# Performance work log

Hardware: AMD Instinct MI355X
Metric: run time of the kernel (lower is better)

Reference implementation:

```python
import jax, jax.numpy as jnp
import numpy as np

N = 100000      # total nodes across the batch of graphs
E = 1600000     # total edges (avg degree 16)
D = 128         # dim_drug (== num_feature here)
L = 3           # layer_drug
G = 2048        # number of graphs in the batch
BN_EPS = 1e-5


def setup_inputs() -> dict:
    key = jax.random.key(0)
    ks = jax.random.split(key, 10)
    x = jax.random.normal(ks[0], (N, D), dtype=jnp.float32)
    edge_index = jax.random.randint(ks[1], (2, E), 0, N, dtype=jnp.int64)
    batch = jnp.sort(jax.random.randint(ks[2], (N,), 0, G, dtype=jnp.int64))
    s = 0.05
    W1 = jax.random.normal(ks[3], (L, D, D), dtype=jnp.float32) * s
    b1 = jax.random.normal(ks[4], (L, D), dtype=jnp.float32) * s
    W2 = jax.random.normal(ks[5], (L, D, D), dtype=jnp.float32) * s
    b2 = jax.random.normal(ks[6], (L, D), dtype=jnp.float32) * s
    gamma = jnp.ones((L, D), dtype=jnp.float32)
    beta = jnp.zeros((L, D), dtype=jnp.float32)
    return {"x": x, "edge_index": edge_index, "batch": batch,
            "W1": W1, "b1": b1, "W2": W2, "b2": b2,
            "gamma": gamma, "beta": beta}


def reference(x, edge_index, batch, W1, b1, W2, b2, gamma, beta):
    src, dst = edge_index[0], edge_index[1]
    h = x
    layer_outs = []
    for i in range(L):
        # GINConv, eps=0: MLP( (1+eps)*h + sum_{j->i} h_j )
        agg = jax.ops.segment_sum(h[src], dst, num_segments=N)  # [N, D]
        m = agg + h
        m = jax.nn.relu(m @ W1[i] + b1[i]) @ W2[i] + b2[i]       # 2-layer MLP
        m = jax.nn.relu(m)                                        # F.relu after conv
        # BatchNorm1d (training mode: batch stats over node dim, biased var)
        mean = jnp.mean(m, axis=0)
        var = jnp.mean((m - mean) ** 2, axis=0)
        h = gamma[i] * (m - mean) * jax.lax.rsqrt(var + BN_EPS) + beta[i]
        layer_outs.append(h)
    node_rep = jnp.concatenate(layer_outs, axis=1)  # JK 'cat' -> [N, L*D]
    return jax.ops.segment_max(node_rep, batch, num_segments=G)  # [G, L*D]
```

## Files before the change

kernel.cpp:

```cpp
#include <hip/hip_runtime.h>
#include <stdint.h>

#define NN 100000
#define NE 1600000
#define DD 128
#define NL 3
#define NG 2048
#define BN_EPS 1e-5f
#define CAP 56
#define NXCD 8
#define WIN 12500

typedef short s16x8 __attribute__((ext_vector_type(8)));
typedef float f32x4 __attribute__((ext_vector_type(4)));

__device__ __forceinline__ unsigned short f2bfu(float f) {
    union { float f; unsigned int i; } x; x.f = f;
    unsigned int r = x.i + 0x7fffu + ((x.i >> 16) & 1u);
    return (unsigned short)(r >> 16);
}
__device__ __forceinline__ float bfu2f(unsigned short u) {
    union { unsigned int i; float f; } x; x.i = ((unsigned int)u) << 16; return x.f;
}
__device__ __forceinline__ float uplo(unsigned int u) {
    union { unsigned int i; float f; } x; x.i = u << 16; return x.f;
}
__device__ __forceinline__ float uphi(unsigned int u) {
    union { unsigned int i; float f; } x; x.i = u & 0xffff0000u; return x.f;
}
__device__ __forceinline__ void add8(float* a, uint4 v) {
    a[0] += uplo(v.x); a[1] += uphi(v.x);
    a[2] += uplo(v.y); a[3] += uphi(v.y);
    a[4] += uplo(v.z); a[5] += uphi(v.z);
    a[6] += uplo(v.w); a[7] += uphi(v.w);
}
__device__ __forceinline__ unsigned int pack2(float a, float b) {
    return (unsigned int)f2bfu(a) | ((unsigned int)f2bfu(b) << 16);
}

__global__ __launch_bounds__(256) void k_cvt(
    const float* __restrict__ x, unsigned short* __restrict__ hb)
{
    int i = (blockIdx.x * 256 + threadIdx.x) * 4;
    if (i >= NN * DD) return;
    float4 v = *(const float4*)(x + i);
    ushort4 o;
    o.x = f2bfu(v.x); o.y = f2bfu(v.y); o.z = f2bfu(v.z); o.w = f2bfu(v.w);
    *(ushort4*)(hb + i) = o;
}

__global__ __launch_bounds__(256) void k_wtrans(
    const float* __restrict__ W1, const float* __restrict__ W2,
    unsigned short* __restrict__ Wt)
{
    int idx = blockIdx.x * 256 + threadIdx.x;
    if (idx >= 6 * DD * DD) return;
    int mat = idx >> 14;
    int r = idx & 16383;
    int n = r >> 7, k = r & 127;
    const float* src = (mat < 3) ? (W1 + mat * DD * DD) : (W2 + (mat - 3) * DD * DD);
    Wt[idx] = f2bfu(src[k * DD + n]);
}

__global__ __launch_bounds__(256) void k_bounds(
    const int* __restrict__ batch, int* __restrict__ start)
{
    int n = blockIdx.x * 256 + threadIdx.x;
    if (n >= NN) return;
    int bn = batch[n];
    bn = bn < 0 ? 0 : (bn > NG - 1 ? NG - 1 : bn);
    int bp;
    if (n == 0) bp = -1;
    else {
        bp = batch[n - 1];
        bp = bp < 0 ? 0 : (bp > NG - 1 ? NG - 1 : bp);
    }
    for (int g = bp + 1; g <= bn; ++g) start[g] = n;
    if (n == NN - 1) {
        for (int g = bn + 1; g <= NG; ++g) start[g] = NN;
    }
}

__global__ __launch_bounds__(256) void k_fill2(
    const int* __restrict__ ei, int* __restrict__ cnt, int* __restrict__ csr)
{
    const int xcd = blockIdx.x & 7;
    const int slice = blockIdx.x >> 3;
    const int wlo = xcd * WIN, whi = wlo + WIN;
    int e0 = (slice * 256 + threadIdx.x) * 4;
    if (e0 >= NE) return;
    int4 d4 = *(const int4*)(ei + NE + e0);
    int dd[4] = {d4.x, d4.y, d4.z, d4.w};
    bool any = false;
    #pragma unroll
    for (int i = 0; i < 4; ++i)
        any |= (dd[i] >= wlo && dd[i] < whi);
    if (!any) return;
    int4 s4 = *(const int4*)(ei + e0);
    int ss[4] = {s4.x, s4.y, s4.z, s4.w};
    #pragma unroll
    for (int i = 0; i < 4; ++i) {
        int src = ss[i], dst = dd[i];
        if (dst < wlo || dst >= whi) continue;
        if ((unsigned)src >= NN) continue;
        int pos = atomicAdd(&cnt[dst], 1);
        if (pos < CAP) csr[dst * CAP + pos] = src;
    }
}

__global__ __launch_bounds__(256) void k_agg(
    const unsigned short* __restrict__ hb, const int* __restrict__ cnt,
    const int* __restrict__ csr, unsigned short* __restrict__ aggf)
{
    const int node = blockIdx.x * 16 + (threadIdx.x >> 4);
    const int lane = threadIdx.x & 15;
    if (node >= NN) return;
    int deg = cnt[node];
    deg = deg > CAP ? CAP : deg;
    const int* bkt = csr + node * CAP;
    const unsigned short* base = hb + lane * 8;
    float acc[8];
    {
        uint4 v = *(const uint4*)(base + (long long)node * DD);
        acc[0] = uplo(v.x); acc[1] = uphi(v.x);
        acc[2] = uplo(v.y); acc[3] = uphi(v.y);
        acc[4] = uplo(v.z); acc[5] = uphi(v.z);
        acc[6] = uplo(v.w); acc[7] = uphi(v.w);
    }
    int e = 0;
    for (; e + 4 <= deg; e += 4) {
        int s0 = bkt[e], s1 = bkt[e + 1], s2 = bkt[e + 2], s3 = bkt[e + 3];
        uint4 v0 = *(const uint4*)(base + (long long)s0 * DD);
        uint4 v1 = *(const uint4*)(base + (long long)s1 * DD);
        uint4 v2 = *(const uint4*)(base + (long long)s2 * DD);
        uint4 v3 = *(const uint4*)(base + (long long)s3 * DD);
        add8(acc, v0); add8(acc, v1); add8(acc, v2); add8(acc, v3);
    }
    for (; e < deg; ++e) {
        uint4 v = *(const uint4*)(base + (long long)bkt[e] * DD);
        add8(acc, v);
    }
    uint4 o;
    o.x = pack2(acc[0], acc[1]);
    o.y = pack2(acc[2], acc[3]);
    o.z = pack2(acc[4], acc[5]);
    o.w = pack2(acc[6], acc[7]);
    *(uint4*)(aggf + (long long)node * DD + lane * 8) = o;
}

__global__ __launch_bounds__(256, 2) void k_mlp(
    const unsigned short* __restrict__ aggf, unsigned short* __restrict__ hb,
    const unsigned short* __restrict__ W1t, const float* __restrict__ b1,
    const unsigned short* __restrict__ W2t, const float* __restrict__ b2,
    float* __restrict__ stats)
{
    __shared__ unsigned short lA[128 * 136];
    __shared__ unsigned short lW[128 * 136];
    __shared__ float sSum[4][128];
    __shared__ float sSq[4][128];
    const int tid = threadIdx.x;
    const int row0 = blockIdx.x * 128;

    #pragma unroll
    for (int it = 0; it < 8; ++it) {
        int eidx = (it * 256 + tid) * 8;
        int r = eidx >> 7, c = eidx & 127;
        *(uint4*)(&lW[r * 136 + c]) = *(const uint4*)(W1t + eidx);
    }
    {
        int col8 = tid & 15, rr = tid >> 4;
        #pragma unroll
        for (int it = 0; it < 8; ++it) {
            int r = rr + it * 16;
            int grow = row0 + r;
            uint4 v;
            if (grow < NN) {
                v = *(const uint4*)(aggf + (long long)grow * DD + col8 * 8);
            } else {
                v.x = v.y = v.z = v.w = 0;
            }
            *(uint4*)(&lA[r * 136 + col8 * 8]) = v;
        }
    }
    __syncthreads();

    const int wave = tid >> 6, lane = tid & 63;
    const int quad = lane >> 4, m16 = lane & 15;

    f32x4 acc[2][8] = {};
    #pragma unroll
    for (int k0 = 0; k0 < 128; k0 += 32) {
        const int kk = k0 + quad * 8;
        s16x8 a0 = *(const s16x8*)(&lA[(wave * 32 + m16) * 136 + kk]);
        s16x8 a1 = *(const s16x8*)(&lA[(wave * 32 + 16 + m16) * 136 + kk]);
        #pragma unroll
        for (int ct = 0; ct < 8; ++ct) {
            s16x8 bf = *(const s16x8*)(&lW[(ct * 16 + m16) * 136 + kk]);
            acc[0][ct] = __builtin_amdgcn_mfma_f32_16x16x32_bf16(a0, bf, acc[0][ct], 0, 0, 0);
            acc[1][ct] = __builtin_amdgcn_mfma_f32_16x16x32_bf16(a1, bf, acc[1][ct], 0, 0, 0);
        }
    }
    __syncthreads();

    #pragma unroll
    for (int rt = 0; rt < 2; ++rt) {
        #pragma unroll
        for (int ct = 0; ct < 8; ++ct) {
            int col = ct * 16 + m16;
            float b = b1[col];
            #pragma unroll
            for (int r = 0; r < 4; ++r) {
                int lrow = wave * 32 + rt * 16 + quad * 4 + r;
                lA[lrow * 136 + col] = f2bfu(fmaxf(acc[rt][ct][r] + b, 0.0f));
            }
        }
    }
    #pragma unroll
    for (int it = 0; it < 8; ++it) {
        int eidx = (it * 256 + tid) * 8;
        int r = eidx >> 7, c = eidx & 127;
        *(uint4*)(&lW[r * 136 + c]) = *(const uint4*)(W2t + eidx);
    }
    __syncthreads();

    #pragma unroll
    for (int rt = 0; rt < 2; ++rt)
        #pragma unroll
        for (int ct = 0; ct < 8; ++ct)
            acc[rt][ct] = f32x4{0.f, 0.f, 0.f, 0.f};
    #pragma unroll
    for (int k0 = 0; k0 < 128; k0 += 32) {
        const int kk = k0 + quad * 8;
        s16x8 a0 = *(const s16x8*)(&lA[(wave * 32 + m16) * 136 + kk]);
        s16x8 a1 = *(const s16x8*)(&lA[(wave * 32 + 16 + m16) * 136 + kk]);
        #pragma unroll
        for (int ct = 0; ct < 8; ++ct) {
            s16x8 bf = *(const s16x8*)(&lW[(ct * 16 + m16) * 136 + kk]);
            acc[0][ct] = __builtin_amdgcn_mfma_f32_16x16x32_bf16(a0, bf, acc[0][ct], 0, 0, 0);
            acc[1][ct] = __builtin_amdgcn_mfma_f32_16x16x32_bf16(a1, bf, acc[1][ct], 0, 0, 0);
        }
    }

    float csum[8] = {}, csq[8] = {};
    #pragma unroll
    for (int rt = 0; rt < 2; ++rt) {
        int rbase = row0 + wave * 32 + rt * 16 + quad * 4;
        #pragma unroll
        for (int ct = 0; ct < 8; ++ct) {
            int col = ct * 16 + m16;
            float b = b2[col];
            #pragma unroll
            for (int r = 0; r < 4; ++r) {
                int row = rbase + r;
                if (row < NN) {
                    float v = fmaxf(acc[rt][ct][r] + b, 0.0f);
                    hb[(long long)row * DD + col] = f2bfu(v);
                    csum[ct] += v;
                    csq[ct] += v * v;
                }
            }
        }
    }
    #pragma unroll
    for (int ct = 0; ct < 8; ++ct) {
        csum[ct] += __shfl_xor(csum[ct], 16);
        csum[ct] += __shfl_xor(csum[ct], 32);
        csq[ct]  += __shfl_xor(csq[ct], 16);
        csq[ct]  += __shfl_xor(csq[ct], 32);
    }
    if (quad == 0) {
        #pragma unroll
        for (int ct = 0; ct < 8; ++ct) {
            int col = ct * 16 + m16;
            sSum[wave][col] = csum[ct];
            sSq[wave][col] = csq[ct];
        }
    }
    __syncthreads();
    if (tid < 128) {
        float s = sSum[0][tid] + sSum[1][tid] + sSum[2][tid] + sSum[3][tid];
        float q = sSq[0][tid] + sSq[1][tid] + sSq[2][tid] + sSq[3][tid];
        atomicAdd(&stats[tid], s);
        atomicAdd(&stats[DD + tid], q);
    }
}

__global__ __launch_bounds__(128) void k_norm(
    unsigned short* __restrict__ hb, const float* __restrict__ stats,
    const float* __restrict__ gamma, const float* __restrict__ beta,
    const int* __restrict__ start, float* __restrict__ out, int layer)
{
    const int d = threadIdx.x;
    const int g = blockIdx.x;
    const float inv_n = 1.0f / (float)NN;
    float mean = stats[d] * inv_n;
    float var = stats[DD + d] * inv_n - mean * mean;
    float inv = rsqrtf(fmaxf(var, 0.f) + BN_EPS);
    float ga = gamma[d];
    float be = beta[d];
    int n0 = start[g], n1 = start[g + 1];
    n0 = n0 < 0 ? 0 : (n0 > NN ? NN : n0);
    n1 = n1 < 0 ? 0 : (n1 > NN ? NN : n1);
    float mx = -3.0e38f;
    int n = n0;
    for (; n + 2 <= n1; n += 2) {
        float v0 = bfu2f(hb[(long long)n * DD + d]);
        float v1 = bfu2f(hb[(long long)(n + 1) * DD + d]);
        float h0 = ga * (v0 - mean) * inv + be;
        float h1 = ga * (v1 - mean) * inv + be;
        hb[(long long)n * DD + d] = f2bfu(h0);
        hb[(long long)(n + 1) * DD + d] = f2bfu(h1);
        mx = fmaxf(mx, fmaxf(h0, h1));
    }
    if (n < n1) {
        float v = bfu2f(hb[(long long)n * DD + d]);
        float hv = ga * (v - mean) * inv + be;
        hb[(long long)n * DD + d] = f2bfu(hv);
        mx = fmaxf(mx, hv);
    }
    if (n1 <= n0) mx = 0.f;
    out[(long long)g * (NL * DD) + layer * DD + d] = mx;
}

extern "C" void kernel_launch(void* const* d_in, const int* in_sizes, int n_in,
                              void* d_out, int out_size, void* d_ws, size_t ws_size,
                              hipStream_t stream) {
    const float* x     = (const float*)d_in[0];
    const int*   ei    = (const int*)d_in[1];
    const int*   batch = (const int*)d_in[2];
    const float* W1    = (const float*)d_in[3];
    const float* b1    = (const float*)d_in[4];
    const float* W2    = (const float*)d_in[5];
    const float* b2    = (const float*)d_in[6];
    const float* gamma = (const float*)d_in[7];
    const float* beta  = (const float*)d_in[8];
    float* out = (float*)d_out;
    unsigned short* aggf = (unsigned short*)d_in[0];

    char* p = (char*)d_ws;
    float*          stats = (float*)p;
    int*            cnt   = (int*)(p + 4096);
    int*            start = (int*)(p + 405504);
    unsigned short* Wt    = (unsigned short*)(p + 417792);
    int*            csr   = (int*)(p + 614400);
    unsigned short* hb    = (unsigned short*)(p + 23014400);

    hipMemsetAsync(p, 0, 404096, stream);
    k_cvt<<<(NN * DD / 4 + 255) / 256, 256, 0, stream>>>(x, hb);
    k_wtrans<<<(6 * DD * DD + 255) / 256, 256, 0, stream>>>(W1, W2, Wt);
    k_bounds<<<(NN + 255) / 256, 256, 0, stream>>>(batch, start);
    {
        int slices = (NE / 4 + 255) / 256;
        k_fill2<<<slices * NXCD, 256, 0, stream>>>(ei, cnt, csr);
    }

    for (int l = 0; l < NL; ++l) {
        float* stats_l = stats + l * 256;
        k_agg<<<(NN + 15) / 16, 256, 0, stream>>>(hb, cnt, csr, aggf);
        k_mlp<<<(NN + 127) / 128, 256, 0, stream>>>(aggf, hb,
                                                    Wt + l * DD * DD, b1 + l * DD,
                                                    Wt + (3 + l) * DD * DD, b2 + l * DD,
                                                    stats_l);
        k_norm<<<NG, 128, 0, stream>>>(hb, stats_l, gamma + l * DD, beta + l * DD,
                                       start, out, l);
    }
}
```

Baseline: 544.1 us.

## Fuse neighbor aggregation into MLP kernel and ping-pong feature buffers

Result: slower. 605.9 us (+11.4%).

```diff
diff --git a/kernel.cpp b/kernel.cpp
--- a/kernel.cpp
+++ b/kernel.cpp
@@ -89,15 +89,23 @@
     const int wlo = xcd * WIN, whi = wlo + WIN;
     int e0 = (slice * 256 + threadIdx.x) * 4;
     if (e0 >= NE) return;
-    int4 d4 = *(const int4*)(ei + NE + e0);
-    int dd[4] = {d4.x, d4.y, d4.z, d4.w};
+    const int* dp = ei + NE + e0;
+    int dd[4];
+    dd[0] = __builtin_nontemporal_load(dp + 0);
+    dd[1] = __builtin_nontemporal_load(dp + 1);
+    dd[2] = __builtin_nontemporal_load(dp + 2);
+    dd[3] = __builtin_nontemporal_load(dp + 3);
     bool any = false;
     #pragma unroll
     for (int i = 0; i < 4; ++i)
         any |= (dd[i] >= wlo && dd[i] < whi);
     if (!any) return;
-    int4 s4 = *(const int4*)(ei + e0);
-    int ss[4] = {s4.x, s4.y, s4.z, s4.w};
+    const int* sp = ei + e0;
+    int ss[4];
+    ss[0] = __builtin_nontemporal_load(sp + 0);
+    ss[1] = __builtin_nontemporal_load(sp + 1);
+    ss[2] = __builtin_nontemporal_load(sp + 2);
+    ss[3] = __builtin_nontemporal_load(sp + 3);
     #pragma unroll
     for (int i = 0; i < 4; ++i) {
         int src = ss[i], dst = dd[i];
@@ -108,48 +116,9 @@
     }
 }
 
-__global__ __launch_bounds__(256) void k_agg(
-    const unsigned short* __restrict__ hb, const int* __restrict__ cnt,
-    const int* __restrict__ csr, unsigned short* __restrict__ aggf)
-{
-    const int node = blockIdx.x * 16 + (threadIdx.x >> 4);
-    const int lane = threadIdx.x & 15;
-    if (node >= NN) return;
-    int deg = cnt[node];
-    deg = deg > CAP ? CAP : deg;
-    const int* bkt = csr + node * CAP;
-    const unsigned short* base = hb + lane * 8;
-    float acc[8];
-    {
-        uint4 v = *(const uint4*)(base + (long long)node * DD);
-        acc[0] = uplo(v.x); acc[1] = uphi(v.x);
-        acc[2] = uplo(v.y); acc[3] = uphi(v.y);
-        acc[4] = uplo(v.z); acc[5] = uphi(v.z);
-        acc[6] = uplo(v.w); acc[7] = uphi(v.w);
-    }
-    int e = 0;
-    for (; e + 4 <= deg; e += 4) {
-        int s0 = bkt[e], s1 = bkt[e + 1], s2 = bkt[e + 2], s3 = bkt[e + 3];
-        uint4 v0 = *(const uint4*)(base + (long long)s0 * DD);
-        uint4 v1 = *(const uint4*)(base + (long long)s1 * DD);
-        uint4 v2 = *(const uint4*)(base + (long long)s2 * DD);
-        uint4 v3 = *(const uint4*)(base + (long long)s3 * DD);
-        add8(acc, v0); add8(acc, v1); add8(acc, v2); add8(acc, v3);
-    }
-    for (; e < deg; ++e) {
-        uint4 v = *(const uint4*)(base + (long long)bkt[e] * DD);
-        add8(acc, v);
-    }
-    uint4 o;
-    o.x = pack2(acc[0], acc[1]);
-    o.y = pack2(acc[2], acc[3]);
-    o.z = pack2(acc[4], acc[5]);
-    o.w = pack2(acc[6], acc[7]);
-    *(uint4*)(aggf + (long long)node * DD + lane * 8) = o;
-}
-
 __global__ __launch_bounds__(256, 2) void k_mlp(
-    const unsigned short* __restrict__ aggf, unsigned short* __restrict__ hb,
+    const unsigned short* __restrict__ hin, unsigned short* __restrict__ hout,
+    const int* __restrict__ cnt, const int* __restrict__ csr,
     const unsigned short* __restrict__ W1t, const float* __restrict__ b1,
     const unsigned short* __restrict__ W2t, const float* __restrict__ b2,
     float* __restrict__ stats)
@@ -168,18 +137,41 @@
         *(uint4*)(&lW[r * 136 + c]) = *(const uint4*)(W1t + eidx);
     }
     {
-        int col8 = tid & 15, rr = tid >> 4;
-        #pragma unroll
+        const int lane = tid & 15;
+        const unsigned short* base = hin + lane * 8;
         for (int it = 0; it < 8; ++it) {
-            int r = rr + it * 16;
-            int grow = row0 + r;
-            uint4 v;
-            if (grow < NN) {
-                v = *(const uint4*)(aggf + (long long)grow * DD + col8 * 8);
-            } else {
-                v.x = v.y = v.z = v.w = 0;
+            int r = it * 16 + (tid >> 4);
+            int node = row0 + r;
+            float acc[8] = {0.f, 0.f, 0.f, 0.f, 0.f, 0.f, 0.f, 0.f};
+            if (node < NN) {
+                uint4 v = *(const uint4*)(base + (long long)node * DD);
+                acc[0] = uplo(v.x); acc[1] = uphi(v.x);
+                acc[2] = uplo(v.y); acc[3] = uphi(v.y);
+                acc[4] = uplo(v.z); acc[5] = uphi(v.z);
+                acc[6] = uplo(v.w); acc[7] = uphi(v.w);
+                int deg = cnt[node];
+                deg = deg > CAP ? CAP : deg;
+                const int* bkt = csr + node * CAP;
+                int e = 0;
+                for (; e + 4 <= deg; e += 4) {
+                    int s0 = bkt[e], s1 = bkt[e + 1], s2 = bkt[e + 2], s3 = bkt[e + 3];
+                    uint4 v0 = *(const uint4*)(base + (long long)s0 * DD);
+                    uint4 v1 = *(const uint4*)(base + (long long)s1 * DD);
+                    uint4 v2 = *(const uint4*)(base + (long long)s2 * DD);
+                    uint4 v3 = *(const uint4*)(base + (long long)s3 * DD);
+                    add8(acc, v0); add8(acc, v1); add8(acc, v2); add8(acc, v3);
+                }
+                for (; e < deg; ++e) {
+                    uint4 v2 = *(const uint4*)(base + (long long)bkt[e] * DD);
+                    add8(acc, v2);
+                }
             }
-            *(uint4*)(&lA[r * 136 + col8 * 8]) = v;
+            uint4 o;
+            o.x = pack2(acc[0], acc[1]);
+            o.y = pack2(acc[2], acc[3]);
+            o.z = pack2(acc[4], acc[5]);
+            o.w = pack2(acc[6], acc[7]);
+            *(uint4*)(&lA[r * 136 + lane * 8]) = o;
         }
     }
     __syncthreads();
@@ -254,7 +246,7 @@
                 int row = rbase + r;
                 if (row < NN) {
                     float v = fmaxf(acc[rt][ct][r] + b, 0.0f);
-                    hb[(long long)row * DD + col] = f2bfu(v);
+                    hout[(long long)row * DD + col] = f2bfu(v);
                     csum[ct] += v;
                     csq[ct] += v * v;
                 }
@@ -285,41 +277,39 @@
     }
 }
 
-__global__ __launch_bounds__(128) void k_norm(
+template <bool WR>
+__global__ __launch_bounds__(256) void k_norm(
     unsigned short* __restrict__ hb, const float* __restrict__ stats,
     const float* __restrict__ gamma, const float* __restrict__ beta,
     const int* __restrict__ start, float* __restrict__ out, int layer)
 {
-    const int d = threadIdx.x;
+    __shared__ float sMx[256];
+    const int d = threadIdx.x & 127;
+    const int half = threadIdx.x >> 7;
     const int g = blockIdx.x;
     const float inv_n = 1.0f / (float)NN;
     float mean = stats[d] * inv_n;
     float var = stats[DD + d] * inv_n - mean * mean;
     float inv = rsqrtf(fmaxf(var, 0.f) + BN_EPS);
-    float ga = gamma[d];
-    float be = beta[d];
+    float a = gamma[d] * inv;
+    float c = beta[d] - mean * a;
     int n0 = start[g], n1 = start[g + 1];
     n0 = n0 < 0 ? 0 : (n0 > NN ? NN : n0);
     n1 = n1 < 0 ? 0 : (n1 > NN ? NN : n1);
     float mx = -3.0e38f;
-    int n = n0;
-    for (; n + 2 <= n1; n += 2) {
-        float v0 = bfu2f(hb[(long long)n * DD + d]);
-        float v1 = bfu2f(hb[(long long)(n + 1) * DD + d]);
-        float h0 = ga * (v0 - mean) * inv + be;
-        float h1 = ga * (v1 - mean) * inv + be;
-        hb[(long long)n * DD + d] = f2bfu(h0);
-        hb[(long long)(n + 1) * DD + d] = f2bfu(h1);
-        mx = fmaxf(mx, fmaxf(h0, h1));
-    }
-    if (n < n1) {
+    for (int n = n0 + half; n < n1; n += 2) {
         float v = bfu2f(hb[(long long)n * DD + d]);
-        float hv = ga * (v - mean) * inv + be;
-        hb[(long long)n * DD + d] = f2bfu(hv);
+        float hv = a * v + c;
+        if (WR) hb[(long long)n * DD + d] = f2bfu(hv);
         mx = fmaxf(mx, hv);
     }
-    if (n1 <= n0) mx = 0.f;
-    out[(long long)g * (NL * DD) + layer * DD + d] = mx;
+    sMx[threadIdx.x] = mx;
+    __syncthreads();
+    if (threadIdx.x < 128) {
+        float m = fmaxf(sMx[d], sMx[d + 128]);
+        if (n1 <= n0) m = 0.f;
+        out[(long long)g * (NL * DD) + layer * DD + d] = m;
+    }
 }
 
 extern "C" void kernel_launch(void* const* d_in, const int* in_sizes, int n_in,
@@ -335,7 +325,7 @@
     const float* gamma = (const float*)d_in[7];
     const float* beta  = (const float*)d_in[8];
     float* out = (float*)d_out;
-    unsigned short* aggf = (unsigned short*)d_in[0];
+    unsigned short* hb1 = (unsigned short*)d_in[0];
 
     char* p = (char*)d_ws;
     float*          stats = (float*)p;
@@ -343,10 +333,10 @@
     int*            start = (int*)(p + 405504);
     unsigned short* Wt    = (unsigned short*)(p + 417792);
     int*            csr   = (int*)(p + 614400);
-    unsigned short* hb    = (unsigned short*)(p + 23014400);
+    unsigned short* hb0   = (unsigned short*)(p + 23014400);
 
     hipMemsetAsync(p, 0, 404096, stream);
-    k_cvt<<<(NN * DD / 4 + 255) / 256, 256, 0, stream>>>(x, hb);
+    k_cvt<<<(NN * DD / 4 + 255) / 256, 256, 0, stream>>>(x, hb0);
     k_wtrans<<<(6 * DD * DD + 255) / 256, 256, 0, stream>>>(W1, W2, Wt);
     k_bounds<<<(NN + 255) / 256, 256, 0, stream>>>(batch, start);
     {
@@ -356,12 +346,17 @@
 
     for (int l = 0; l < NL; ++l) {
         float* stats_l = stats + l * 256;
-        k_agg<<<(NN + 15) / 16, 256, 0, stream>>>(hb, cnt, csr, aggf);
-        k_mlp<<<(NN + 127) / 128, 256, 0, stream>>>(aggf, hb,
+        unsigned short* hin  = (l & 1) ? hb1 : hb0;
+        unsigned short* hout = (l & 1) ? hb0 : hb1;
+        k_mlp<<<(NN + 127) / 128, 256, 0, stream>>>(hin, hout, cnt, csr,
                                                     Wt + l * DD * DD, b1 + l * DD,
                                                     Wt + (3 + l) * DD * DD, b2 + l * DD,
                                                     stats_l);
-        k_norm<<<NG, 128, 0, stream>>>(hb, stats_l, gamma + l * DD, beta + l * DD,
-                                       start, out, l);
-    }
-}
+        if (l < NL - 1)
+            k_norm<true><<<NG, 256, 0, stream>>>(hout, stats_l, gamma + l * DD,
+                                                 beta + l * DD, start, out, l);
+        else
+            k_norm<false><<<NG, 256, 0, stream>>>(hout, stats_l, gamma + l * DD,
+                                                  beta + l * DD, start, out, l);
+    }
+}
```
